# Optimization experiments

Measured on AMD Instinct MI355X. Metric: run time of the kernel, lower is better.

Reference implementation:

```python
import jax, jax.numpy as jnp
import numpy as np

INPUT_DIM = 1024
HIDDEN = 1024
OUTPUT = 512
LAYERS = 3
BATCH = 2048
ALPHA = 0.5
EPS = 0.01


def _orthogonal(rng, n):
    # torch init: orthogonal_ * 0.8, then spectral_norm divides by sigma (=0.8),
    # so the effective forward weight is exactly orthogonal.
    q, _ = np.linalg.qr(rng.standard_normal((n, n)))
    return q.astype(np.float32)


def setup_inputs() -> dict:
    rng = np.random.default_rng(0)
    x = jnp.asarray(rng.standard_normal((BATCH, INPUT_DIM)).astype(np.float32))
    # embed: Linear(input_dim, hidden_dim); weight [out, in]
    We = jnp.asarray((rng.standard_normal((HIDDEN, INPUT_DIM)) / np.sqrt(INPUT_DIM)).astype(np.float32))
    be = jnp.asarray((rng.standard_normal(HIDDEN) * 0.01).astype(np.float32))
    # recurrent layers: spectral-normalized [H,H] weights (effectively orthogonal)
    W = jnp.asarray(np.stack([_orthogonal(rng, HIDDEN) for _ in range(LAYERS)]))  # [L,H,H]
    b = jnp.asarray((rng.standard_normal((LAYERS, HIDDEN)) * 0.01).astype(np.float32))
    # head: Linear(hidden_dim, output_dim)
    Wh = jnp.asarray((rng.standard_normal((OUTPUT, HIDDEN)) / np.sqrt(HIDDEN)).astype(np.float32))
    bh = jnp.asarray((rng.standard_normal(OUTPUT) * 0.01).astype(np.float32))
    return {"x": x, "We": We, "be": be, "W": W, "b": b, "Wh": Wh, "bh": bh, "steps": 30}


def reference(x, We, be, W, b, Wh, bh, steps):
    # x: [B, I]; We: [H, I]; W: [L, H, H]; Wh: [O, H]
    x_emb = x @ We.T + be  # [B, H]
    L = W.shape[0]
    B = x.shape[0]
    H = W.shape[1]
    h0 = jnp.zeros((L, B, H), dtype=x.dtype)
    prev0 = jnp.zeros((L, B, H), dtype=x.dtype)

    def step(carry, _):
        h, prev = carry  # both [L, B, H], states/prev_inputs from previous step
        # layer 0 sees x_emb; layer i>0 sees previous-step state of layer i-1
        inputs = jnp.concatenate([x_emb[None], h[:-1]], axis=0)  # [L, B, H]
        # activity gate: mean |delta input| over features > epsilon
        mask = (jnp.mean(jnp.abs(inputs - prev), axis=-1, keepdims=True) > EPS).astype(x.dtype)  # [L,B,1]
        h_new = jnp.tanh(jnp.einsum('lbi,loi->lbo', inputs, W) + b[:, None, :])  # [L,B,H]
        h_upd = (1.0 - ALPHA) * h + ALPHA * h_new
        h_out = mask * h_upd + (1.0 - mask) * h
        return (h_out, inputs), None

    (h_final, _), _ = jax.lax.scan(step, (h0, prev0), None, length=steps)
    return h_final[-1] @ Wh.T + bh  # [B, O]
```

## Files before the change

kernel.cpp:

```cpp
#include <hip/hip_runtime.h>
#include <math.h>


using half_t = _Float16;
typedef _Float16 f16x4 __attribute__((ext_vector_type(4)));
typedef _Float16 f16x8 __attribute__((ext_vector_type(8)));
typedef float    f32x4 __attribute__((ext_vector_type(4)));

constexpr int KDIM = 1024;
constexpr int ROWB = KDIM * 2;
constexpr float EPS_GATE = 0.01f;

__device__ __forceinline__ float tanh_fast(float z) {
    return 1.0f - 2.0f / (__expf(2.0f * z) + 1.0f);
}

__device__ __forceinline__ void gload16(const void* g, void* l) {
    __builtin_amdgcn_global_load_lds(
        (const __attribute__((address_space(1))) void*)g,
        (__attribute__((address_space(3))) void*)l, 16, 0, 0);
}

__global__ __launch_bounds__(256)
void convert_all(const float* __restrict__ x,  const float* __restrict__ We,
                 const float* __restrict__ W,  const float* __restrict__ Wh,
                 half_t* __restrict__ x16, half_t* __restrict__ We16,
                 half_t* __restrict__ W16, half_t* __restrict__ Wh16,
                 float* __restrict__ msum) {
    const int bid = blockIdx.x;
    const int t = threadIdx.x;
    if (bid < 6) ((f32x4*)msum)[bid * 256 + t] = f32x4{0.f, 0.f, 0.f, 0.f};
    const float* src; half_t* dst; int row;
    if (bid < 2048)      { src = x;  dst = x16;  row = bid; }
    else if (bid < 3072) { src = We; dst = We16; row = bid - 2048; }
    else if (bid < 6144) { src = W;  dst = W16;  row = bid - 3072; }
    else                 { src = Wh; dst = Wh16; row = bid - 6144; }
    const f32x4 v = *(const f32x4*)(src + (size_t)row * KDIM + 4 * t);
    f16x4 h;
    h[0] = (half_t)v[0]; h[1] = (half_t)v[1]; h[2] = (half_t)v[2]; h[3] = (half_t)v[3];
    const int p = (8 * t) ^ ((row & 7) << 4);
    *(f16x4*)((char*)dst + (size_t)row * ROWB + p) = h;
}

template <int EPI, bool EMIT>
__global__ __launch_bounds__(512)
void gemm8w(const half_t* __restrict__ P, const half_t* __restrict__ Q,
            const float* __restrict__ bias, const float* __restrict__ msum_in,
            float* __restrict__ msum_out, void* __restrict__ Out, int Nout) {
    __shared__ alignas(16) char smem[3 * 24576];

    const int tid = threadIdx.x;
    const int bid = blockIdx.x;
    const int m0 = ((bid & 7) * 2 + ((bid >> 3) & 1)) * 128;
    const int n0 = (bid >> 4) * 64;

    const char* gP0 = (const char*)P + (size_t)(m0 + (tid >> 3)) * ROWB + (tid & 7) * 16;
    const char* gP1 = gP0 + (size_t)64 * ROWB;
    const char* gQ  = (const char*)Q + (size_t)(n0 + (tid >> 3)) * ROWB + (tid & 7) * 16;
    const int ldsT = tid * 16;

    const int lane = tid & 63;
    const int w = tid >> 6;
    const int wm = (w & 3) * 32;
    const int wn = (w >> 2) * 32;
    const int l15 = lane & 15, l4 = lane >> 4;
    const int off0 = (l4 * 16) ^ ((lane & 7) << 4);
    const int off1 = off0 ^ 64;

    f32x4 acc[2][2] = {};

    auto stage = [&](int s) {
        const int go = s * 128;
        char* base = smem + (s % 3) * 24576;
        gload16(gP0 + go, base + ldsT);
        gload16(gP1 + go, base + 8192 + ldsT);
        gload16(gQ + go, base + 16384 + ldsT);
    };

    stage(0);
    stage(1);

    for (int s = 0; s < 16; ++s) {
        if (s == 15) asm volatile("s_waitcnt vmcnt(0)" ::: "memory");
        else         asm volatile("s_waitcnt vmcnt(3)" ::: "memory");
        __builtin_amdgcn_s_barrier();
        asm volatile("" ::: "memory");
        if (s < 14) stage(s + 2);
        const char* PtB = smem + (s % 3) * 24576;
        const char* QtB = PtB + 16384;
        __builtin_amdgcn_s_setprio(1);
#pragma unroll
        for (int h = 0; h < 2; ++h) {
            const int ko = h ? off1 : off0;
            f16x8 qa[2], pb[2];
#pragma unroll
            for (int i = 0; i < 2; ++i)
                qa[i] = *(const f16x8*)(QtB + (wn + i * 16 + l15) * 128 + ko);
#pragma unroll
            for (int j = 0; j < 2; ++j)
                pb[j] = *(const f16x8*)(PtB + (wm + j * 16 + l15) * 128 + ko);
#pragma unroll
            for (int i = 0; i < 2; ++i)
#pragma unroll
                for (int j = 0; j < 2; ++j)
                    acc[i][j] = __builtin_amdgcn_mfma_f32_16x16x32_f16(qa[i], pb[j], acc[i][j], 0, 0, 0);
        }
        __builtin_amdgcn_s_setprio(0);
    }

#pragma unroll
    for (int j = 0; j < 2; ++j) {
        const int m = m0 + wm + j * 16 + l15;
        float msk = 1.0f;
        if (EPI == 1) msk = (msum_in[m] * (1.0f / 1024.0f) > EPS_GATE) ? 1.0f : 0.0f;
        float rsum = 0.0f;
#pragma unroll
        for (int i = 0; i < 2; ++i) {
            const int n = n0 + wn + i * 16 + l4 * 4;
            const f32x4 bz = *(const f32x4*)(bias + n);
            float v[4];
#pragma unroll
            for (int e = 0; e < 4; ++e) {
                v[e] = acc[i][j][e] + bz[e];
                if (EPI == 1) v[e] = msk * (0.5f * tanh_fast(v[e]));
                if (EMIT) rsum += fabsf(v[e]);
            }
            if (EPI == 2) {
                f32x4 o; o[0] = v[0]; o[1] = v[1]; o[2] = v[2]; o[3] = v[3];
                *(f32x4*)((float*)Out + (size_t)m * Nout + n) = o;
            } else {
                f16x4 hv;
                hv[0] = (half_t)v[0]; hv[1] = (half_t)v[1];
                hv[2] = (half_t)v[2]; hv[3] = (half_t)v[3];
                const int p = (n * 2) ^ ((m & 7) << 4);
                *(f16x4*)((char*)Out + (size_t)m * ROWB + p) = hv;
            }
        }
        if (EMIT) {
            rsum += __shfl_xor(rsum, 16, 64);
            rsum += __shfl_xor(rsum, 32, 64);
            if (l4 == 0) atomicAdd(msum_out + m, rsum);
        }
    }
}

template <int EPI, bool EMIT>
__global__ __launch_bounds__(256)
void gemm2b(const half_t* __restrict__ P, const half_t* __restrict__ Q,
            const float* __restrict__ bias, const float* __restrict__ msum_in,
            float* __restrict__ msum_out, void* __restrict__ Out, int Nout) {
    __shared__ alignas(16) char smem[3 * 16384];

    const int tid = threadIdx.x;
    const int bid = blockIdx.x;
    const int m0 = ((bid & 7) * 4 + ((bid >> 3) & 3)) * 64;
    const int n0 = (bid >> 5) * 64;

    const char* gsP[2]; int ldP[2];
#pragma unroll
    for (int i = 0; i < 2; ++i) {
        const int G = tid + 256 * i;
        gsP[i] = (const char*)P + (size_t)(m0 + (G >> 3)) * ROWB + (G & 7) * 16;
        ldP[i] = G * 16;
    }
    const char* gsQ[2]; int ldQ[2];
#pragma unroll
    for (int c = 0; c < 2; ++c) {
        const int g = tid + 256 * c;
        gsQ[c] = (const char*)Q + (size_t)(n0 + (g >> 3)) * ROWB + (g & 7) * 16;
        ldQ[c] = 8192 + g * 16;
    }

    const int lane = tid & 63;
    const int w = tid >> 6;
    const int wm = (w & 1) * 32;
    const int wn = (w >> 1) * 32;
    const int l15 = lane & 15, l4 = lane >> 4;
    const int off0 = (l4 * 16) ^ ((lane & 7) << 4);
    const int off1 = off0 ^ 64;

    f32x4 acc[2][2] = {};

    auto stage = [&](int s) {
        const int go = s * 128;
        char* base = smem + (s % 3) * 16384;
#pragma unroll
        for (int i = 0; i < 2; ++i) gload16(gsP[i] + go, base + ldP[i]);
#pragma unroll
        for (int c = 0; c < 2; ++c) gload16(gsQ[c] + go, base + ldQ[c]);
    };

    stage(0);
    stage(1);

    for (int s = 0; s < 16; ++s) {
        if (s == 15) asm volatile("s_waitcnt vmcnt(0)" ::: "memory");
        else         asm volatile("s_waitcnt vmcnt(4)" ::: "memory");
        __builtin_amdgcn_s_barrier();
        asm volatile("" ::: "memory");
        if (s < 14) stage(s + 2);
        const char* PtB = smem + (s % 3) * 16384;
        const char* QtB = PtB + 8192;
        __builtin_amdgcn_s_setprio(1);
#pragma unroll
        for (int h = 0; h < 2; ++h) {
            const int ko = h ? off1 : off0;
            f16x8 qa[2], pb[2];
#pragma unroll
            for (int i = 0; i < 2; ++i)
                qa[i] = *(const f16x8*)(QtB + (wn + i * 16 + l15) * 128 + ko);
#pragma unroll
            for (int j = 0; j < 2; ++j)
                pb[j] = *(const f16x8*)(PtB + (wm + j * 16 + l15) * 128 + ko);
#pragma unroll
            for (int i = 0; i < 2; ++i)
#pragma unroll
                for (int j = 0; j < 2; ++j)
                    acc[i][j] = __builtin_amdgcn_mfma_f32_16x16x32_f16(qa[i], pb[j], acc[i][j], 0, 0, 0);
        }
        __builtin_amdgcn_s_setprio(0);
    }

#pragma unroll
    for (int j = 0; j < 2; ++j) {
        const int m = m0 + wm + j * 16 + l15;
        float msk = 1.0f;
        if (EPI == 1) msk = (msum_in[m] * (1.0f / 1024.0f) > EPS_GATE) ? 1.0f : 0.0f;
        float rsum = 0.0f;
#pragma unroll
        for (int i = 0; i < 2; ++i) {
            const int n = n0 + wn + i * 16 + l4 * 4;
            const f32x4 bz = *(const f32x4*)(bias + n);
            float v[4];
#pragma unroll
            for (int e = 0; e < 4; ++e) {
                v[e] = acc[i][j][e] + bz[e];
                if (EPI == 1) v[e] = msk * (0.5f * tanh_fast(v[e]));
                if (EMIT) rsum += fabsf(v[e]);
            }
            if (EPI == 2) {
                f32x4 o; o[0] = v[0]; o[1] = v[1]; o[2] = v[2]; o[3] = v[3];
                *(f32x4*)((float*)Out + (size_t)m * Nout + n) = o;
            } else {
                f16x4 hv;
                hv[0] = (half_t)v[0]; hv[1] = (half_t)v[1];
                hv[2] = (half_t)v[2]; hv[3] = (half_t)v[3];
                const int p = (n * 2) ^ ((m & 7) << 4);
                *(f16x4*)((char*)Out + (size_t)m * ROWB + p) = hv;
            }
        }
        if (EMIT) {
            rsum += __shfl_xor(rsum, 16, 64);
            rsum += __shfl_xor(rsum, 32, 64);
            if (l4 == 0) atomicAdd(msum_out + m, rsum);
        }
    }
}

extern "C" void kernel_launch(void* const* d_in, const int* in_sizes, int n_in,
                              void* d_out, int out_size, void* d_ws, size_t ws_size,
                              hipStream_t stream) {
    const float* x  = (const float*)d_in[0];
    const float* We = (const float*)d_in[1];
    const float* be = (const float*)d_in[2];
    const float* W  = (const float*)d_in[3];
    const float* b  = (const float*)d_in[4];
    const float* Wh = (const float*)d_in[5];
    const float* bh = (const float*)d_in[6];

    const int B = 2048, H = 1024, O = 512;

    half_t* s0   = (half_t*)d_ws;
    half_t* s1   = s0 + (size_t)B * H;
    half_t* We16 = s1 + (size_t)B * H;
    half_t* W16  = We16 + (size_t)H * H;
    half_t* Wh16 = W16 + (size_t)3 * H * H;
    float*  msum = (float*)(Wh16 + (size_t)O * H);
    float*  out  = (float*)d_out;

    convert_all<<<6656, 256, 0, stream>>>(x, We, W, Wh, s0, We16, W16, Wh16, msum);

    gemm8w<0, true ><<<256, 512, 0, stream>>>(s0, We16, be, nullptr, msum, s1, H);
    gemm8w<1, true ><<<256, 512, 0, stream>>>(s1, W16, b, msum, msum + 2048, s0, H);
    gemm8w<1, true ><<<256, 512, 0, stream>>>(s0, W16 + (size_t)H * H, b + H,
                                              msum + 2048, msum + 4096, s1, H);
    gemm8w<1, false><<<256, 512, 0, stream>>>(s1, W16 + (size_t)2 * H * H, b + 2 * H,
                                              msum + 4096, nullptr, s0, H);
    gemm2b<2, false><<<256, 256, 0, stream>>>(s0, Wh16, bh, nullptr, nullptr, out, O);
}
```

Baseline: 53.73 us.

## Fuse fp32-to-fp16 conversion into embed GEMM and replace atomics with partial sums

Removes the separate convert kernel. The embed GEMM now loads fp32 x and We directly, converts them to fp16 in registers and stages them into LDS through a register double buffer. Extra blocks in the same launch convert the recurrent and head weights to fp16. The per-row activity sums are now written as per-tile partials into a slot array and summed by the consumer, instead of zero-initialised buffers updated with atomicAdd. This saves a launch and the fp16 round trip of x and We. In exchange the embed GEMM loses its async global-to-LDS path, and each consumer row does extra partial-sum reads.

```diff
diff --git a/kernel.cpp b/kernel.cpp
--- a/kernel.cpp
+++ b/kernel.cpp
@@ -21,20 +21,9 @@
         (__attribute__((address_space(3))) void*)l, 16, 0, 0);
 }
 
-__global__ __launch_bounds__(256)
-void convert_all(const float* __restrict__ x,  const float* __restrict__ We,
-                 const float* __restrict__ W,  const float* __restrict__ Wh,
-                 half_t* __restrict__ x16, half_t* __restrict__ We16,
-                 half_t* __restrict__ W16, half_t* __restrict__ Wh16,
-                 float* __restrict__ msum) {
-    const int bid = blockIdx.x;
-    const int t = threadIdx.x;
-    if (bid < 6) ((f32x4*)msum)[bid * 256 + t] = f32x4{0.f, 0.f, 0.f, 0.f};
-    const float* src; half_t* dst; int row;
-    if (bid < 2048)      { src = x;  dst = x16;  row = bid; }
-    else if (bid < 3072) { src = We; dst = We16; row = bid - 2048; }
-    else if (bid < 6144) { src = W;  dst = W16;  row = bid - 3072; }
-    else                 { src = Wh; dst = Wh16; row = bid - 6144; }
+__device__ __forceinline__ void conv_row(const float* __restrict__ src,
+                                         half_t* __restrict__ dst,
+                                         int row, int t) {
     const f32x4 v = *(const f32x4*)(src + (size_t)row * KDIM + 4 * t);
     f16x4 h;
     h[0] = (half_t)v[0]; h[1] = (half_t)v[1]; h[2] = (half_t)v[2]; h[3] = (half_t)v[3];
@@ -42,11 +31,132 @@
     *(f16x4*)((char*)dst + (size_t)row * ROWB + p) = h;
 }
 
-template <int EPI, bool EMIT>
+__device__ __forceinline__ f16x8 cvt8(f32x4 a, f32x4 b) {
+    f16x8 h;
+    h[0] = (half_t)a[0]; h[1] = (half_t)a[1]; h[2] = (half_t)a[2]; h[3] = (half_t)a[3];
+    h[4] = (half_t)b[0]; h[5] = (half_t)b[1]; h[6] = (half_t)b[2]; h[7] = (half_t)b[3];
+    return h;
+}
+
+__device__ __forceinline__ float part_sum(const float* __restrict__ part, int m) {
+    const f32x4* pp = (const f32x4*)(part + (size_t)m * 32);
+    f32x4 t = pp[0] + pp[1] + pp[2] + pp[3] + pp[4] + pp[5] + pp[6] + pp[7];
+    return t[0] + t[1] + t[2] + t[3];
+}
+
+__global__ __launch_bounds__(512)
+void gemmE_rs(const float* __restrict__ x, const float* __restrict__ We,
+              const float* __restrict__ be,
+              const float* __restrict__ Wf, const float* __restrict__ Whf,
+              half_t* __restrict__ W16, half_t* __restrict__ Wh16,
+              float* __restrict__ part0, half_t* __restrict__ Eout) {
+    __shared__ alignas(16) char smem[2 * 24576];
+
+    const int tid = threadIdx.x;
+    const int bid = blockIdx.x;
+
+    if (bid >= 256) {
+        const int bid2 = bid - 256;
+        const int t = tid & 255;
+        const int rh = tid >> 8;
+#pragma unroll
+        for (int q = 0; q < 16; ++q) {
+            const int r = bid2 * 32 + q * 2 + rh;
+            if (r < 3072) conv_row(Wf, W16, r, t);
+            else          conv_row(Whf, Wh16, r - 3072, t);
+        }
+        return;
+    }
+
+    const int m0 = ((bid & 7) * 2 + ((bid >> 3) & 1)) * 128;
+    const int n0 = (bid >> 4) * 64;
+
+    const int srow = tid >> 3;
+    const int g    = tid & 7;
+    const int e8   = (g * 8) ^ ((srow & 7) * 8);
+    const float* gp0 = x  + (size_t)(m0 + srow) * KDIM + e8;
+    const float* gp1 = x  + (size_t)(m0 + 64 + srow) * KDIM + e8;
+    const float* gq  = We + (size_t)(n0 + srow) * KDIM + e8;
+    const int ldsT = tid * 16;
+
+    const int lane = tid & 63;
+    const int w = tid >> 6;
+    const int wm = (w & 3) * 32;
+    const int wn = (w >> 2) * 32;
+    const int l15 = lane & 15, l4 = lane >> 4;
+    const int off0 = (l4 * 16) ^ ((lane & 7) << 4);
+    const int off1 = off0 ^ 64;
+
+    f32x4 rp[6];
+    auto load = [&](int s) {
+        const int o = s * 64;
+        rp[0] = *(const f32x4*)(gp0 + o); rp[1] = *(const f32x4*)(gp0 + o + 4);
+        rp[2] = *(const f32x4*)(gp1 + o); rp[3] = *(const f32x4*)(gp1 + o + 4);
+        rp[4] = *(const f32x4*)(gq  + o); rp[5] = *(const f32x4*)(gq  + o + 4);
+    };
+
+    f32x4 acc[2][2] = {};
+
+    load(0);
+    for (int s = 0; s < 16; ++s) {
+        char* buf = smem + (s & 1) * 24576;
+        *(f16x8*)(buf + ldsT)         = cvt8(rp[0], rp[1]);
+        *(f16x8*)(buf + 8192 + ldsT)  = cvt8(rp[2], rp[3]);
+        *(f16x8*)(buf + 16384 + ldsT) = cvt8(rp[4], rp[5]);
+        __syncthreads();
+        if (s < 15) load(s + 1);
+        const char* PtB = buf;
+        const char* QtB = buf + 16384;
+        __builtin_amdgcn_s_setprio(1);
+#pragma unroll
+        for (int h = 0; h < 2; ++h) {
+            const int ko = h ? off1 : off0;
+            f16x8 qa[2], pb[2];
+#pragma unroll
+            for (int i = 0; i < 2; ++i)
+                qa[i] = *(const f16x8*)(QtB + (wn + i * 16 + l15) * 128 + ko);
+#pragma unroll
+            for (int j = 0; j < 2; ++j)
+                pb[j] = *(const f16x8*)(PtB + (wm + j * 16 + l15) * 128 + ko);
+#pragma unroll
+            for (int i = 0; i < 2; ++i)
+#pragma unroll
+                for (int j = 0; j < 2; ++j)
+                    acc[i][j] = __builtin_amdgcn_mfma_f32_16x16x32_f16(qa[i], pb[j], acc[i][j], 0, 0, 0);
+        }
+        __builtin_amdgcn_s_setprio(0);
+    }
+
+    const int slot = (n0 >> 6) * 2 + (wn >> 5);
+#pragma unroll
+    for (int j = 0; j < 2; ++j) {
+        const int m = m0 + wm + j * 16 + l15;
+        float rsum = 0.0f;
+#pragma unroll
+        for (int i = 0; i < 2; ++i) {
+            const int n = n0 + wn + i * 16 + l4 * 4;
+            const f32x4 bz = *(const f32x4*)(be + n);
+            f16x4 hv;
+#pragma unroll
+            for (int e = 0; e < 4; ++e) {
+                const float v = acc[i][j][e] + bz[e];
+                rsum += fabsf(v);
+                hv[e] = (half_t)v;
+            }
+            const int p = (n * 2) ^ ((m & 7) << 4);
+            *(f16x4*)((char*)Eout + (size_t)m * ROWB + p) = hv;
+        }
+        rsum += __shfl_xor(rsum, 16, 64);
+        rsum += __shfl_xor(rsum, 32, 64);
+        if (l4 == 0) part0[(size_t)m * 32 + slot] = rsum;
+    }
+}
+
+template <bool EMIT>
 __global__ __launch_bounds__(512)
 void gemm8w(const half_t* __restrict__ P, const half_t* __restrict__ Q,
-            const float* __restrict__ bias, const float* __restrict__ msum_in,
-            float* __restrict__ msum_out, void* __restrict__ Out, int Nout) {
+            const float* __restrict__ bias, const float* __restrict__ part_in,
+            float* __restrict__ part_out, half_t* __restrict__ Out) {
     __shared__ alignas(16) char smem[3 * 24576];
 
     const int tid = threadIdx.x;
@@ -108,47 +218,37 @@
         __builtin_amdgcn_s_setprio(0);
     }
 
+    const int slot = (n0 >> 6) * 2 + (wn >> 5);
 #pragma unroll
     for (int j = 0; j < 2; ++j) {
         const int m = m0 + wm + j * 16 + l15;
-        float msk = 1.0f;
-        if (EPI == 1) msk = (msum_in[m] * (1.0f / 1024.0f) > EPS_GATE) ? 1.0f : 0.0f;
+        const float msk = (part_sum(part_in, m) * (1.0f / 1024.0f) > EPS_GATE) ? 1.0f : 0.0f;
         float rsum = 0.0f;
 #pragma unroll
         for (int i = 0; i < 2; ++i) {
             const int n = n0 + wn + i * 16 + l4 * 4;
             const f32x4 bz = *(const f32x4*)(bias + n);
-            float v[4];
+            f16x4 hv;
 #pragma unroll
             for (int e = 0; e < 4; ++e) {
-                v[e] = acc[i][j][e] + bz[e];
-                if (EPI == 1) v[e] = msk * (0.5f * tanh_fast(v[e]));
-                if (EMIT) rsum += fabsf(v[e]);
+                float v = msk * (0.5f * tanh_fast(acc[i][j][e] + bz[e]));
+                if (EMIT) rsum += fabsf(v);
+                hv[e] = (half_t)v;
             }
-            if (EPI == 2) {
-                f32x4 o; o[0] = v[0]; o[1] = v[1]; o[2] = v[2]; o[3] = v[3];
-                *(f32x4*)((float*)Out + (size_t)m * Nout + n) = o;
-            } else {
-                f16x4 hv;
-                hv[0] = (half_t)v[0]; hv[1] = (half_t)v[1];
-                hv[2] = (half_t)v[2]; hv[3] = (half_t)v[3];
-                const int p = (n * 2) ^ ((m & 7) << 4);
-                *(f16x4*)((char*)Out + (size_t)m * ROWB + p) = hv;
-            }
+            const int p = (n * 2) ^ ((m & 7) << 4);
+            *(f16x4*)((char*)Out + (size_t)m * ROWB + p) = hv;
         }
         if (EMIT) {
             rsum += __shfl_xor(rsum, 16, 64);
             rsum += __shfl_xor(rsum, 32, 64);
-            if (l4 == 0) atomicAdd(msum_out + m, rsum);
-        }
-    }
-}
-
-template <int EPI, bool EMIT>
+            if (l4 == 0) part_out[(size_t)m * 32 + slot] = rsum;
+        }
+    }
+}
+
 __global__ __launch_bounds__(256)
-void gemm2b(const half_t* __restrict__ P, const half_t* __restrict__ Q,
-            const float* __restrict__ bias, const float* __restrict__ msum_in,
-            float* __restrict__ msum_out, void* __restrict__ Out, int Nout) {
+void gemm_head(const half_t* __restrict__ P, const half_t* __restrict__ Q,
+               const float* __restrict__ bias, float* __restrict__ Out) {
     __shared__ alignas(16) char smem[3 * 16384];
 
     const int tid = threadIdx.x;
@@ -166,9 +266,9 @@
     const char* gsQ[2]; int ldQ[2];
 #pragma unroll
     for (int c = 0; c < 2; ++c) {
-        const int g = tid + 256 * c;
-        gsQ[c] = (const char*)Q + (size_t)(n0 + (g >> 3)) * ROWB + (g & 7) * 16;
-        ldQ[c] = 8192 + g * 16;
+        const int gg = tid + 256 * c;
+        gsQ[c] = (const char*)Q + (size_t)(n0 + (gg >> 3)) * ROWB + (gg & 7) * 16;
+        ldQ[c] = 8192 + gg * 16;
     }
 
     const int lane = tid & 63;
@@ -224,35 +324,14 @@
 #pragma unroll
     for (int j = 0; j < 2; ++j) {
         const int m = m0 + wm + j * 16 + l15;
-        float msk = 1.0f;
-        if (EPI == 1) msk = (msum_in[m] * (1.0f / 1024.0f) > EPS_GATE) ? 1.0f : 0.0f;
-        float rsum = 0.0f;
 #pragma unroll
         for (int i = 0; i < 2; ++i) {
             const int n = n0 + wn + i * 16 + l4 * 4;
             const f32x4 bz = *(const f32x4*)(bias + n);
-            float v[4];
-#pragma unroll
-            for (int e = 0; e < 4; ++e) {
-                v[e] = acc[i][j][e] + bz[e];
-                if (EPI == 1) v[e] = msk * (0.5f * tanh_fast(v[e]));
-                if (EMIT) rsum += fabsf(v[e]);
-            }
-            if (EPI == 2) {
-                f32x4 o; o[0] = v[0]; o[1] = v[1]; o[2] = v[2]; o[3] = v[3];
-                *(f32x4*)((float*)Out + (size_t)m * Nout + n) = o;
-            } else {
-                f16x4 hv;
-                hv[0] = (half_t)v[0]; hv[1] = (half_t)v[1];
-                hv[2] = (half_t)v[2]; hv[3] = (half_t)v[3];
-                const int p = (n * 2) ^ ((m & 7) << 4);
-                *(f16x4*)((char*)Out + (size_t)m * ROWB + p) = hv;
-            }
-        }
-        if (EMIT) {
-            rsum += __shfl_xor(rsum, 16, 64);
-            rsum += __shfl_xor(rsum, 32, 64);
-            if (l4 == 0) atomicAdd(msum_out + m, rsum);
+            f32x4 o;
+#pragma unroll
+            for (int e = 0; e < 4; ++e) o[e] = acc[i][j][e] + bz[e];
+            *(f32x4*)(Out + (size_t)m * 512 + n) = o;
         }
     }
 }
@@ -270,21 +349,20 @@
 
     const int B = 2048, H = 1024, O = 512;
 
-    half_t* s0   = (half_t*)d_ws;
-    half_t* s1   = s0 + (size_t)B * H;
-    half_t* We16 = s1 + (size_t)B * H;
-    half_t* W16  = We16 + (size_t)H * H;
-    half_t* Wh16 = W16 + (size_t)3 * H * H;
-    float*  msum = (float*)(Wh16 + (size_t)O * H);
-    float*  out  = (float*)d_out;
-
-    convert_all<<<6656, 256, 0, stream>>>(x, We, W, Wh, s0, We16, W16, Wh16, msum);
-
-    gemm8w<0, true ><<<256, 512, 0, stream>>>(s0, We16, be, nullptr, msum, s1, H);
-    gemm8w<1, true ><<<256, 512, 0, stream>>>(s1, W16, b, msum, msum + 2048, s0, H);
-    gemm8w<1, true ><<<256, 512, 0, stream>>>(s0, W16 + (size_t)H * H, b + H,
-                                              msum + 2048, msum + 4096, s1, H);
-    gemm8w<1, false><<<256, 512, 0, stream>>>(s1, W16 + (size_t)2 * H * H, b + 2 * H,
-                                              msum + 4096, nullptr, s0, H);
-    gemm2b<2, false><<<256, 256, 0, stream>>>(s0, Wh16, bh, nullptr, nullptr, out, O);
-}
+    half_t* s0    = (half_t*)d_ws;
+    half_t* s1    = s0 + (size_t)B * H;
+    half_t* W16   = s1 + (size_t)B * H;
+    half_t* Wh16  = W16 + (size_t)3 * H * H;
+    float*  part0 = (float*)(Wh16 + (size_t)O * H);
+    float*  part1 = part0 + 65536;
+    float*  part2 = part1 + 65536;
+    float*  out   = (float*)d_out;
+
+    gemmE_rs<<<368, 512, 0, stream>>>(x, We, be, W, Wh, W16, Wh16, part0, s1);
+    gemm8w<true ><<<256, 512, 0, stream>>>(s1, W16, b, part0, part1, s0);
+    gemm8w<true ><<<256, 512, 0, stream>>>(s0, W16 + (size_t)H * H, b + H,
+                                           part1, part2, s1);
+    gemm8w<false><<<256, 512, 0, stream>>>(s1, W16 + (size_t)2 * H * H, b + 2 * H,
+                                           part2, nullptr, s0);
+    gemm_head<<<256, 256, 0, stream>>>(s0, Wh16, bh, out);
+}
```

After: 62.87 us. 1.17x slower.
